# Optimization experiments

Hardware: AMD Instinct MI355X
Metric: run time of the kernel (lower is better)

## Reference

```python
import jax, jax.numpy as jnp
import numpy as np
from jax import lax


def _gauss1d(size, sigma):
    k = np.arange(size, dtype=np.float32) - (size - 1) / 2.0
    k = np.exp(-0.5 * (k / sigma) ** 2)
    return k / k.sum()


def _make_kernel(scale, sigma):
    # make_odd
    kx, ky, kz = [s + 1 if s % 2 == 0 else s for s in scale]
    kH = _gauss1d(kx, sigma)
    kW = _gauss1d(ky, sigma)
    kD = _gauss1d(kz, sigma)
    kern = kH[:, None, None] * kW[None, :, None] * kD[None, None, :]  # (kx, ky, kz)
    kern = np.transpose(kern, (2, 0, 1))  # permute(2,0,1) -> (kz, kx, ky)
    return jnp.asarray(kern, dtype=jnp.float32)


def setup_inputs() -> dict:
    key = jax.random.key(0)
    x = jax.random.normal(key, (2, 1, 256, 256, 256), dtype=jnp.float32)
    kernel0 = _make_kernel((2, 2, 2), 1.0)  # (3,3,3)
    kernel1 = _make_kernel((4, 4, 4), 1.0)  # (5,5,5)
    return {"x": x, "kernel0": kernel0, "kernel1": kernel1}


def _blur_down(x, kernel, stride):
    # replicate pad by k//2 per spatial dim, then depthwise (C=1) conv3d.
    pad = [(0, 0), (0, 0)] + [(k // 2, k // 2) for k in kernel.shape]
    xp = jnp.pad(x, pad, mode='edge')
    # strided VALID conv == full blur followed by [::s] slicing (output ceil(H/s))
    return lax.conv_general_dilated(
        xp, kernel[None, None].astype(x.dtype),
        window_strides=stride, padding='VALID',
        dimension_numbers=('NCDHW', 'OIDHW', 'NCDHW'))


def reference(x, kernel0, kernel1):
    d1 = _blur_down(x, kernel0, (2, 2, 2))  # (2,1,128,128,128)
    d2 = _blur_down(x, kernel1, (4, 4, 4))  # (2,1,64,64,64)
    return (x, d1, d2)
```

## Files before the change

kernel.cpp:

```cpp
#include <hip/hip_runtime.h>

#define S_IN 256
#define IN_PER_BATCH (S_IN * S_IN * S_IN)
#define D1_PER_BATCH (128 * 128 * 128)
#define D2_PER_BATCH (64 * 64 * 64)
#define X_ELEMS (2 * IN_PER_BATCH)
#define D1_ELEMS (2 * D1_PER_BATCH)
#define D2_ELEMS (2 * D2_PER_BATCH)

#define LXR 40
#define NROW 144
#define BUFV 1536
#define BUFF (BUFV * 4)
#define TPB 8
#define NBLK 2048

__device__ __forceinline__ void gload_lds16(const float* g, float* l) {
    __builtin_amdgcn_global_load_lds(
        (const __attribute__((address_space(1))) void*)g,
        (__attribute__((address_space(3))) void*)l, 16, 0, 0);
}

__global__ __launch_bounds__(256) void fused_pyramid(
    const float* __restrict__ x, const float* __restrict__ k0,
    const float* __restrict__ k1, float* __restrict__ out0,
    float* __restrict__ out1, float* __restrict__ out2)
{
    __shared__ float ls[2 * BUFF];
    __shared__ float kw0[9][4];
    __shared__ float kw1[25][8];

    const int tid = threadIdx.x;
    if (tid < 27) kw0[tid / 3][tid % 3] = k0[tid];
    else if (tid >= 32 && tid < 157) {
        int t = tid - 32;
        kw1[t / 5][t % 5] = k1[t];
    }

    const int bid  = blockIdx.x;
    const int wt   = bid & 7;
    const int hy   = (bid >> 3) & 31;
    const int dzn0 = bid >> 8;
    const int x0 = wt << 5;
    const int y0 = hy << 3;
    const bool edge = (wt == 0);

    int gcol[6];
    int lzo[6];
#pragma unroll
    for (int i = 0; i < 6; ++i) {
        int v = tid + (i << 8);
        int row = v / 10;
        int j = v - row * 10;
        int lz = row / 12;
        int ly = row - lz * 12;
        int gy = y0 + ly - 2; gy = gy < 0 ? 0 : (gy > 255 ? 255 : gy);
        int gx = x0 - 4 + (j << 2); gx = gx < 0 ? 0 : (gx > 252 ? 252 : gx);
        gcol[i] = (gy << 8) + gx;
        lzo[i] = lz - 2;
    }

    const bool pact = edge && (tid < NROW);
    int plz = 0, ply = 0, pgy = 0;
    if (pact) {
        plz = tid / 12;
        ply = tid - plz * 12;
        int gy = y0 + ply - 2; pgy = gy < 0 ? 0 : (gy > 255 ? 255 : gy);
    }
    float pv = 0.0f;

    auto issue_dma = [&](int dzn, int buf) {
        const int z0 = (dzn & 31) << 3;
        const float* xb = x + (size_t)(dzn >> 5) * IN_PER_BATCH;
        float* lb = ls + buf * BUFF + (tid << 2);
#pragma unroll
        for (int i = 0; i < 6; ++i) {
            int gz = z0 + lzo[i]; gz = gz < 0 ? 0 : (gz > 255 ? 255 : gz);
            gload_lds16(xb + (((size_t)gz << 16) + gcol[i]), lb + (size_t)i * 1024);
        }
    };
    auto patch_load = [&](int dzn) {
        if (pact) {
            int z0 = (dzn & 31) << 3;
            int gz = z0 + plz - 2; gz = gz < 0 ? 0 : (gz > 255 ? 255 : gz);
            pv = x[(size_t)(dzn >> 5) * IN_PER_BATCH + ((size_t)gz << 16) + (pgy << 8)];
        }
    };
    auto patch_write = [&](int buf) {
        if (pact) {
            *reinterpret_cast<float2*>(
                &ls[buf * BUFF + (plz * 12 + ply) * LXR + 2]) = make_float2(pv, pv);
        }
    };

    auto compute = [&](int dzn, int buf) {
        const int dz = dzn & 31;
        const int n  = dzn >> 5;
        const float* B = ls + buf * BUFF;

        {
            float* ob0 = out0 + (size_t)n * IN_PER_BATCH
                       + (((size_t)dz << 3) << 16) + (y0 << 8) + x0;
#pragma unroll
            for (int k = 0; k < 2; ++k) {
                int v = tid + (k << 8);
                int jj = v & 7;
                int rowc = v >> 3;
                int lzc = rowc >> 3, lyc = rowc & 7;
                float4 val = *reinterpret_cast<const float4*>(
                    &B[((lzc + 2) * 12 + (lyc + 2)) * LXR + 4 + (jj << 2)]);
                *reinterpret_cast<float4*>(
                    &ob0[((size_t)lzc << 16) + (lyc << 8) + (jj << 2)]) = val;
            }
        }

        {
            const int ox = tid & 15, oy = (tid >> 4) & 3, oz = tid >> 6;
            const float* base = B + ((2 * oz + 1) * 12 + (2 * oy + 1)) * LXR + 2 * ox + 2;
            float acc = 0.0f;
#pragma unroll
            for (int a = 0; a < 3; ++a)
#pragma unroll
                for (int b = 0; b < 3; ++b) {
                    const float* lr = base + (a * 12 + b) * LXR;
                    float2 v0 = *reinterpret_cast<const float2*>(lr);
                    float2 v1 = *reinterpret_cast<const float2*>(lr + 2);
                    float4 kr = *reinterpret_cast<const float4*>(&kw0[a * 3 + b][0]);
                    acc = fmaf(kr.x, v0.y, acc);
                    acc = fmaf(kr.y, v1.x, acc);
                    acc = fmaf(kr.z, v1.y, acc);
                }
            float* ob1 = out1 + (size_t)n * D1_PER_BATCH
                       + (((size_t)dz << 2) << 14) + ((hy << 2) << 7) + (wt << 4);
            ob1[(oz << 14) + (oy << 7) + ox] = acc;
        }

        {
            const int q = tid & 7;
            const int o = tid >> 3;
            const int ox = o & 7, oy = (o >> 3) & 1, oz = o >> 4;
            float acc = 0.0f;
#pragma unroll
            for (int m = 0; m < 4; ++m) {
                int r = q + (m << 3);
                if (r < 25) {
                    int a = r / 5, b = r - 5 * a;
                    const float* lr = B + ((4 * oz + a) * 12 + (4 * oy + b)) * LXR + 4 * ox;
                    float4 A4 = *reinterpret_cast<const float4*>(lr);
                    float4 B4 = *reinterpret_cast<const float4*>(lr + 4);
                    float4 kr = *reinterpret_cast<const float4*>(&kw1[r][0]);
                    float k4 = kw1[r][4];
                    acc = fmaf(kr.x, A4.z, acc);
                    acc = fmaf(kr.y, A4.w, acc);
                    acc = fmaf(kr.z, B4.x, acc);
                    acc = fmaf(kr.w, B4.y, acc);
                    acc = fmaf(k4,   B4.z, acc);
                }
            }
            acc += __shfl_xor(acc, 1);
            acc += __shfl_xor(acc, 2);
            acc += __shfl_xor(acc, 4);
            if (q == 0) {
                float* ob2 = out2 + (size_t)n * D2_PER_BATCH
                           + (((size_t)dz << 1) << 12) + ((hy << 1) << 6) + (wt << 3);
                ob2[(oz << 12) + (oy << 6) + ox] = acc;
            }
        }
    };

    issue_dma(dzn0, 0);
    if (edge) patch_load(dzn0);
    __syncthreads();
    if (edge) { patch_write(0); __syncthreads(); }

    for (int it = 0; it < TPB; ++it) {
        const int cur = it & 1;
        if (it + 1 < TPB) {
            issue_dma(dzn0 + 8 * (it + 1), cur ^ 1);
            if (edge) patch_load(dzn0 + 8 * (it + 1));
        }
        compute(dzn0 + 8 * it, cur);
        __syncthreads();
        if (edge && it + 1 < TPB) { patch_write(cur ^ 1); __syncthreads(); }
    }
}

extern "C" void kernel_launch(void* const* d_in, const int* in_sizes, int n_in,
                              void* d_out, int out_size, void* d_ws, size_t ws_size,
                              hipStream_t stream) {
    const float* x  = (const float*)d_in[0];
    const float* k0 = (const float*)d_in[1];
    const float* k1 = (const float*)d_in[2];

    float* out0 = (float*)d_out;
    float* out1 = out0 + X_ELEMS;
    float* out2 = out1 + D1_ELEMS;

    fused_pyramid<<<NBLK, 256, 0, stream>>>(x, k0, k1, out0, out1, out2);
}
```

Before: 296.0 us.

## Replace persistent double-buffered loop with one-tile-per-block launch and XCD-aware block mapping

Each block previously walked 8 depth tiles, double-buffering global-to-LDS loads in the background. Now every block handles a single tile with a single LDS buffer, the grid grows to 16384 blocks, and launch bounds ask for 6 blocks per CU. Block indices are remapped so that consecutive hardware block IDs spread across groups (bx&7 picks a 2048-block chunk), which likely targets locality across the XCDs. Latency is now hidden by running many resident blocks rather than by in-block prefetch, at the cost of block launch overhead and of reloading the halo for every tile.

Measured after the change: 294.4 us. Within noise of the previous version (-0.5%).

```diff
diff --git a/kernel.cpp b/kernel.cpp
--- a/kernel.cpp
+++ b/kernel.cpp
@@ -12,8 +12,7 @@
 #define NROW 144
 #define BUFV 1536
 #define BUFF (BUFV * 4)
-#define TPB 8
-#define NBLK 2048
+#define NBLK 16384
 
 __device__ __forceinline__ void gload_lds16(const float* g, float* l) {
     __builtin_amdgcn_global_load_lds(
@@ -21,12 +20,12 @@
         (__attribute__((address_space(3))) void*)l, 16, 0, 0);
 }
 
-__global__ __launch_bounds__(256) void fused_pyramid(
+__global__ __launch_bounds__(256, 6) void fused_pyramid(
     const float* __restrict__ x, const float* __restrict__ k0,
     const float* __restrict__ k1, float* __restrict__ out0,
     float* __restrict__ out1, float* __restrict__ out2)
 {
-    __shared__ float ls[2 * BUFF];
+    __shared__ float ls[BUFF];
     __shared__ float kw0[9][4];
     __shared__ float kw1[25][8];
 
@@ -37,151 +36,123 @@
         kw1[t / 5][t % 5] = k1[t];
     }
 
-    const int bid  = blockIdx.x;
-    const int wt   = bid & 7;
-    const int hy   = (bid >> 3) & 31;
-    const int dzn0 = bid >> 8;
+    const int bx  = blockIdx.x;
+    const int lin = (bx & 7) * 2048 + (bx >> 3);
+    const int wt = lin & 7;
+    const int hy = (lin >> 3) & 31;
+    const int dz = (lin >> 8) & 31;
+    const int n  = lin >> 13;
+
     const int x0 = wt << 5;
     const int y0 = hy << 3;
+    const int z0 = dz << 3;
     const bool edge = (wt == 0);
 
-    int gcol[6];
-    int lzo[6];
+    const float* xb = x + (size_t)n * IN_PER_BATCH;
+
+    {
+        float* lb = ls + (tid << 2);
 #pragma unroll
-    for (int i = 0; i < 6; ++i) {
-        int v = tid + (i << 8);
-        int row = v / 10;
-        int j = v - row * 10;
-        int lz = row / 12;
-        int ly = row - lz * 12;
-        int gy = y0 + ly - 2; gy = gy < 0 ? 0 : (gy > 255 ? 255 : gy);
-        int gx = x0 - 4 + (j << 2); gx = gx < 0 ? 0 : (gx > 252 ? 252 : gx);
-        gcol[i] = (gy << 8) + gx;
-        lzo[i] = lz - 2;
+        for (int i = 0; i < 6; ++i) {
+            int v = tid + (i << 8);
+            int row = v / 10;
+            int j = v - row * 10;
+            int lz = row / 12;
+            int ly = row - lz * 12;
+            int gz = z0 + lz - 2; gz = gz < 0 ? 0 : (gz > 255 ? 255 : gz);
+            int gy = y0 + ly - 2; gy = gy < 0 ? 0 : (gy > 255 ? 255 : gy);
+            int gx = x0 - 4 + (j << 2); gx = gx < 0 ? 0 : (gx > 252 ? 252 : gx);
+            gload_lds16(xb + (((size_t)gz << 16) + (gy << 8) + gx),
+                        lb + (size_t)i * 1024);
+        }
     }
 
+    float pv = 0.0f;
+    int plz = 0, ply = 0;
     const bool pact = edge && (tid < NROW);
-    int plz = 0, ply = 0, pgy = 0;
     if (pact) {
         plz = tid / 12;
         ply = tid - plz * 12;
-        int gy = y0 + ply - 2; pgy = gy < 0 ? 0 : (gy > 255 ? 255 : gy);
+        int gz = z0 + plz - 2; gz = gz < 0 ? 0 : (gz > 255 ? 255 : gz);
+        int gy = y0 + ply - 2; gy = gy < 0 ? 0 : (gy > 255 ? 255 : gy);
+        pv = xb[((size_t)gz << 16) + (gy << 8)];
     }
-    float pv = 0.0f;
 
-    auto issue_dma = [&](int dzn, int buf) {
-        const int z0 = (dzn & 31) << 3;
-        const float* xb = x + (size_t)(dzn >> 5) * IN_PER_BATCH;
-        float* lb = ls + buf * BUFF + (tid << 2);
+    __syncthreads();
+    if (edge) {
+        if (pact)
+            *reinterpret_cast<float2*>(
+                &ls[(plz * 12 + ply) * LXR + 2]) = make_float2(pv, pv);
+        __syncthreads();
+    }
+
+    {
+        float* ob0 = out0 + (size_t)n * IN_PER_BATCH
+                   + (((size_t)dz << 3) << 16) + (y0 << 8) + x0;
 #pragma unroll
-        for (int i = 0; i < 6; ++i) {
-            int gz = z0 + lzo[i]; gz = gz < 0 ? 0 : (gz > 255 ? 255 : gz);
-            gload_lds16(xb + (((size_t)gz << 16) + gcol[i]), lb + (size_t)i * 1024);
+        for (int k = 0; k < 2; ++k) {
+            int v = tid + (k << 8);
+            int jj = v & 7;
+            int rowc = v >> 3;
+            int lzc = rowc >> 3, lyc = rowc & 7;
+            float4 val = *reinterpret_cast<const float4*>(
+                &ls[((lzc + 2) * 12 + (lyc + 2)) * LXR + 4 + (jj << 2)]);
+            *reinterpret_cast<float4*>(
+                &ob0[((size_t)lzc << 16) + (lyc << 8) + (jj << 2)]) = val;
         }
-    };
-    auto patch_load = [&](int dzn) {
-        if (pact) {
-            int z0 = (dzn & 31) << 3;
-            int gz = z0 + plz - 2; gz = gz < 0 ? 0 : (gz > 255 ? 255 : gz);
-            pv = x[(size_t)(dzn >> 5) * IN_PER_BATCH + ((size_t)gz << 16) + (pgy << 8)];
-        }
-    };
-    auto patch_write = [&](int buf) {
-        if (pact) {
-            *reinterpret_cast<float2*>(
-                &ls[buf * BUFF + (plz * 12 + ply) * LXR + 2]) = make_float2(pv, pv);
-        }
-    };
+    }
 
-    auto compute = [&](int dzn, int buf) {
-        const int dz = dzn & 31;
-        const int n  = dzn >> 5;
-        const float* B = ls + buf * BUFF;
+    {
+        const int ox = tid & 15, oy = (tid >> 4) & 3, oz = tid >> 6;
+        const float* base = ls + ((2 * oz + 1) * 12 + (2 * oy + 1)) * LXR + 2 * ox + 2;
+        float acc = 0.0f;
+#pragma unroll
+        for (int a = 0; a < 3; ++a)
+#pragma unroll
+            for (int b = 0; b < 3; ++b) {
+                const float* lr = base + (a * 12 + b) * LXR;
+                float2 v0 = *reinterpret_cast<const float2*>(lr);
+                float2 v1 = *reinterpret_cast<const float2*>(lr + 2);
+                float4 kr = *reinterpret_cast<const float4*>(&kw0[a * 3 + b][0]);
+                acc = fmaf(kr.x, v0.y, acc);
+                acc = fmaf(kr.y, v1.x, acc);
+                acc = fmaf(kr.z, v1.y, acc);
+            }
+        float* ob1 = out1 + (size_t)n * D1_PER_BATCH
+                   + (((size_t)dz << 2) << 14) + ((hy << 2) << 7) + (wt << 4);
+        ob1[(oz << 14) + (oy << 7) + ox] = acc;
+    }
 
-        {
-            float* ob0 = out0 + (size_t)n * IN_PER_BATCH
-                       + (((size_t)dz << 3) << 16) + (y0 << 8) + x0;
+    {
+        const int q = tid & 7;
+        const int o = tid >> 3;
+        const int ox = o & 7, oy = (o >> 3) & 1, oz = o >> 4;
+        float acc = 0.0f;
 #pragma unroll
-            for (int k = 0; k < 2; ++k) {
-                int v = tid + (k << 8);
-                int jj = v & 7;
-                int rowc = v >> 3;
-                int lzc = rowc >> 3, lyc = rowc & 7;
-                float4 val = *reinterpret_cast<const float4*>(
-                    &B[((lzc + 2) * 12 + (lyc + 2)) * LXR + 4 + (jj << 2)]);
-                *reinterpret_cast<float4*>(
-                    &ob0[((size_t)lzc << 16) + (lyc << 8) + (jj << 2)]) = val;
+        for (int m = 0; m < 4; ++m) {
+            int r = q + (m << 3);
+            if (r < 25) {
+                int a = r / 5, b = r - 5 * a;
+                const float* lr = ls + ((4 * oz + a) * 12 + (4 * oy + b)) * LXR + 4 * ox;
+                float4 A4 = *reinterpret_cast<const float4*>(lr);
+                float4 B4 = *reinterpret_cast<const float4*>(lr + 4);
+                float4 kr = *reinterpret_cast<const float4*>(&kw1[r][0]);
+                float k4 = kw1[r][4];
+                acc = fmaf(kr.x, A4.z, acc);
+                acc = fmaf(kr.y, A4.w, acc);
+                acc = fmaf(kr.z, B4.x, acc);
+                acc = fmaf(kr.w, B4.y, acc);
+                acc = fmaf(k4,   B4.z, acc);
             }
         }
-
-        {
-            const int ox = tid & 15, oy = (tid >> 4) & 3, oz = tid >> 6;
-            const float* base = B + ((2 * oz + 1) * 12 + (2 * oy + 1)) * LXR + 2 * ox + 2;
-            float acc = 0.0f;
-#pragma unroll
-            for (int a = 0; a < 3; ++a)
-#pragma unroll
-                for (int b = 0; b < 3; ++b) {
-                    const float* lr = base + (a * 12 + b) * LXR;
-                    float2 v0 = *reinterpret_cast<const float2*>(lr);
-                    float2 v1 = *reinterpret_cast<const float2*>(lr + 2);
-                    float4 kr = *reinterpret_cast<const float4*>(&kw0[a * 3 + b][0]);
-                    acc = fmaf(kr.x, v0.y, acc);
-                    acc = fmaf(kr.y, v1.x, acc);
-                    acc = fmaf(kr.z, v1.y, acc);
-                }
-            float* ob1 = out1 + (size_t)n * D1_PER_BATCH
-                       + (((size_t)dz << 2) << 14) + ((hy << 2) << 7) + (wt << 4);
-            ob1[(oz << 14) + (oy << 7) + ox] = acc;
+        acc += __shfl_xor(acc, 1);
+        acc += __shfl_xor(acc, 2);
+        acc += __shfl_xor(acc, 4);
+        if (q == 0) {
+            float* ob2 = out2 + (size_t)n * D2_PER_BATCH
+                       + (((size_t)dz << 1) << 12) + ((hy << 1) << 6) + (wt << 3);
+            ob2[(oz << 12) + (oy << 6) + ox] = acc;
         }
-
-        {
-            const int q = tid & 7;
-            const int o = tid >> 3;
-            const int ox = o & 7, oy = (o >> 3) & 1, oz = o >> 4;
-            float acc = 0.0f;
-#pragma unroll
-            for (int m = 0; m < 4; ++m) {
-                int r = q + (m << 3);
-                if (r < 25) {
-                    int a = r / 5, b = r - 5 * a;
-                    const float* lr = B + ((4 * oz + a) * 12 + (4 * oy + b)) * LXR + 4 * ox;
-                    float4 A4 = *reinterpret_cast<const float4*>(lr);
-                    float4 B4 = *reinterpret_cast<const float4*>(lr + 4);
-                    float4 kr = *reinterpret_cast<const float4*>(&kw1[r][0]);
-                    float k4 = kw1[r][4];
-                    acc = fmaf(kr.x, A4.z, acc);
-                    acc = fmaf(kr.y, A4.w, acc);
-                    acc = fmaf(kr.z, B4.x, acc);
-                    acc = fmaf(kr.w, B4.y, acc);
-                    acc = fmaf(k4,   B4.z, acc);
-                }
-            }
-            acc += __shfl_xor(acc, 1);
-            acc += __shfl_xor(acc, 2);
-            acc += __shfl_xor(acc, 4);
-            if (q == 0) {
-                float* ob2 = out2 + (size_t)n * D2_PER_BATCH
-                           + (((size_t)dz << 1) << 12) + ((hy << 1) << 6) + (wt << 3);
-                ob2[(oz << 12) + (oy << 6) + ox] = acc;
-            }
-        }
-    };
-
-    issue_dma(dzn0, 0);
-    if (edge) patch_load(dzn0);
-    __syncthreads();
-    if (edge) { patch_write(0); __syncthreads(); }
-
-    for (int it = 0; it < TPB; ++it) {
-        const int cur = it & 1;
-        if (it + 1 < TPB) {
-            issue_dma(dzn0 + 8 * (it + 1), cur ^ 1);
-            if (edge) patch_load(dzn0 + 8 * (it + 1));
-        }
-        compute(dzn0 + 8 * it, cur);
-        __syncthreads();
-        if (edge && it + 1 < TPB) { patch_write(cur ^ 1); __syncthreads(); }
     }
 }
 
```
